# Optimization experiments

Hardware: AMD Instinct MI355X
Metric: run time of the kernel (lower is better)

The kernel has to match this reference:

```python
import jax, jax.numpy as jnp
import numpy as np

N_NODES = 100000
N_EDGES = 1600000
K = 5
C = 32
HEADS = 2
LRELU_GAT = 0.2   # SuperGAT negative_slope default
LRELU_OUT = 0.01  # nn.LeakyReLU default
BN_EPS = 1e-5


def setup_inputs() -> dict:
    key = jax.random.key(0)
    ks = jax.random.split(key, 10)
    patch_embs = jax.random.normal(ks[0], (N_NODES, C), dtype=jnp.float32)
    src = jax.random.randint(ks[1], (N_EDGES,), 0, N_NODES, dtype=jnp.int32)
    dst = jax.random.randint(ks[2], (N_EDGES,), 0, N_NODES, dtype=jnp.int32)
    dst = jnp.where(src == dst, (dst + 1) % N_NODES, dst)  # graph has no self-loops
    edge_index = jnp.stack([src, dst])
    edge_attr = jax.random.normal(ks[3], (N_EDGES, 1), dtype=jnp.float32)
    g = 1.0 / np.sqrt(C).astype(np.float32)
    cheb_w = jax.random.normal(ks[4], (K, C, C), dtype=jnp.float32) * g
    cheb_b = jnp.zeros((C,), jnp.float32)
    lin_w = jax.random.normal(ks[5], (C, HEADS * C), dtype=jnp.float32) * g
    att_l = jax.random.normal(ks[6], (HEADS, C), dtype=jnp.float32) * g
    att_r = jax.random.normal(ks[7], (HEADS, C), dtype=jnp.float32) * g
    gat_b = jnp.zeros((C,), jnp.float32)
    bn_g = jnp.ones((C,), jnp.float32)
    bn_b = jnp.zeros((C,), jnp.float32)
    return dict(patch_embs=patch_embs, edge_index=edge_index, edge_attr=edge_attr,
                cheb_w=cheb_w, cheb_b=cheb_b, lin_w=lin_w, att_l=att_l,
                att_r=att_r, gat_b=gat_b, bn_g=bn_g, bn_b=bn_b)


def cheb_conv(x, src, dst, w_edge, cheb_w, cheb_b, n):
    # PyG ChebConv with sym norm, lambda_max=2: L_hat = -D^-1/2 A D^-1/2
    def prop(t):
        return jax.ops.segment_sum(t[src] * w_edge[:, None], dst, num_segments=n)
    Tx0 = x
    out = Tx0 @ cheb_w[0]
    Tx1 = prop(x)
    out = out + Tx1 @ cheb_w[1]
    for k in range(2, cheb_w.shape[0]):
        Tx2 = 2.0 * prop(Tx1) - Tx0
        out = out + Tx2 @ cheb_w[k]
        Tx0, Tx1 = Tx1, Tx2
    return out + cheb_b


def supergat(x, src, dst, lin_w, att_l, att_r, bias, n):
    # SuperGATConv, attention_type='MX', heads=2, concat=False, with self-loops
    H, Ch = att_l.shape
    h = (x @ lin_w).reshape(n, H, Ch)
    xj = h[src]            # [E, H, C] messages from source
    xi = h[dst]            # [E, H, C] target features
    logits = jnp.sum(xi * xj, axis=-1)                         # [E, H]
    alpha = jnp.sum(xj * att_l, -1) + jnp.sum(xi * att_r, -1)  # [E, H]
    alpha = alpha * jax.nn.sigmoid(logits)
    alpha = jax.nn.leaky_relu(alpha, LRELU_GAT)
    # segment softmax over destination nodes
    m = jax.ops.segment_max(alpha, dst, num_segments=n)
    e = jnp.exp(alpha - m[dst])
    s = jax.ops.segment_sum(e, dst, num_segments=n)
    a = e / s[dst]
    out = jax.ops.segment_sum(xj * a[..., None], dst, num_segments=n)  # [N, H, C]
    return out.mean(axis=1) + bias  # concat=False -> head mean


def reference(patch_embs, edge_index, edge_attr, cheb_w, cheb_b, lin_w, att_l,
              att_r, gat_b, bn_g, bn_b):
    n = patch_embs.shape[0]
    src, dst = edge_index[0], edge_index[1]
    # symmetric Laplacian normalization weights
    deg = jax.ops.segment_sum(jnp.ones_like(src, dtype=patch_embs.dtype), src,
                              num_segments=n)
    dis = jnp.where(deg > 0, jax.lax.rsqrt(jnp.maximum(deg, 1.0)), 0.0)
    w_edge = -dis[src] * dis[dst]
    x = cheb_conv(patch_embs, src, dst, w_edge, cheb_w, cheb_b, n)
    # add self-loops for SuperGAT (PyG default add_self_loops=True)
    loop = jnp.arange(n, dtype=src.dtype)
    src2 = jnp.concatenate([src, loop])
    dst2 = jnp.concatenate([dst, loop])
    x2 = supergat(x, src2, dst2, lin_w, att_l, att_r, gat_b, n)
    # LeakyReLU + residual + BatchNorm1d (training-mode batch stats)
    y = jax.nn.leaky_relu(x2, LRELU_OUT) + x2
    mu = y.mean(axis=0)
    var = ((y - mu) ** 2).mean(axis=0)  # biased variance
    return (y - mu) * jax.lax.rsqrt(var + BN_EPS) * bn_g + bn_b
```

## Files before the change

### kernel.cpp

```cpp
#include <hip/hip_runtime.h>
#include <hip/hip_fp16.h>
#include <math.h>

#define CC 32
#define CHUNK 4096
#define NCPY 16
#define REDB 1024

static inline int cdiv(long long a, int b) { return (int)((a + b - 1) / b); }

__device__ inline float4 h4f(int2 r) {
  __half2 lo = *reinterpret_cast<__half2*>(&r.x);
  __half2 hi = *reinterpret_cast<__half2*>(&r.y);
  float2 a = __half22float2(lo), b = __half22float2(hi);
  return make_float4(a.x, a.y, b.x, b.y);
}

__global__ void k_cnt(const int* __restrict__ src, const int* __restrict__ dst,
                      int* __restrict__ priv, int E, int N) {
  int e = blockIdx.x * blockDim.x + threadIdx.x;
  if (e >= E) return;
  int* p = priv + (size_t)(blockIdx.x & (NCPY - 1)) * N;
  atomicAdd(&p[src[e]], 1 << 16);
  atomicAdd(&p[dst[e]], 1);
}

__global__ void k_reduce(int* __restrict__ priv, float* __restrict__ dis,
                         int* __restrict__ cnt, int* __restrict__ histmat, int N) {
  __shared__ int lh[64];
  if (threadIdx.x < 64) lh[threadIdx.x] = 0;
  __syncthreads();
  int n = blockIdx.x * REDB + threadIdx.x;
  if (n < N) {
    int vals[NCPY];
    int tot = 0;
#pragma unroll
    for (int c = 0; c < NCPY; ++c) {
      vals[c] = priv[(size_t)c * N + n];
      tot += vals[c];
    }
    int deg = tot >> 16, cv = tot & 0xFFFF;
    dis[n] = (deg > 0) ? rsqrtf((float)deg) : 0.f;
    cnt[n] = cv;
    int acc = 0;
#pragma unroll
    for (int c = 0; c < NCPY; ++c) {
      priv[(size_t)c * N + n] = acc;
      acc += vals[c] & 0xFFFF;
    }
    atomicAdd(&lh[min(cv, 63)], 1);
  }
  __syncthreads();
  if (threadIdx.x < 64) histmat[blockIdx.x * 64 + threadIdx.x] = lh[threadIdx.x];
}

__global__ void k_scanhist2(int* __restrict__ histmat, int nb) {
  int lane = threadIdx.x;
  int tot = 0;
  for (int i = 0; i < nb; ++i) tot += histmat[i * 64 + lane];
  __shared__ int sh[64], pf[64];
  sh[lane] = tot;
  __syncthreads();
  if (lane == 0) {
    int acc = 0;
    for (int b = 0; b < 64; ++b) { pf[b] = acc; acc += sh[b]; }
  }
  __syncthreads();
  int acc = pf[lane];
  for (int i = 0; i < nb; ++i) {
    int v = histmat[i * 64 + lane];
    histmat[i * 64 + lane] = acc;
    acc += v;
  }
}

__global__ void k_permfill2(const int* __restrict__ cnt, const int* __restrict__ histmat,
                            int* __restrict__ perm, int N) {
  __shared__ int lh[64], lbase[64];
  if (threadIdx.x < 64) lh[threadIdx.x] = 0;
  __syncthreads();
  int i = blockIdx.x * REDB + threadIdx.x;
  int bin = 0, rank = 0;
  bool act = (i < N);
  if (act) {
    bin = min(cnt[i], 63);
    rank = atomicAdd(&lh[bin], 1);
  }
  __syncthreads();
  if (threadIdx.x < 64) lbase[threadIdx.x] = histmat[blockIdx.x * 64 + threadIdx.x];
  __syncthreads();
  if (act) perm[lbase[bin] + rank] = i;
}

__global__ void k_chunksum(const int* __restrict__ cnt, int* __restrict__ csum, int N) {
  int base = blockIdx.x * CHUNK;
  int v = 0;
  for (int i = threadIdx.x; i < CHUNK; i += 256) {
    int idx = base + i;
    if (idx < N) v += cnt[idx];
  }
  for (int m = 32; m; m >>= 1) v += __shfl_xor(v, m);
  __shared__ int ws[4];
  if ((threadIdx.x & 63) == 0) ws[threadIdx.x >> 6] = v;
  __syncthreads();
  if (threadIdx.x == 0) csum[blockIdx.x] = ws[0] + ws[1] + ws[2] + ws[3];
}

__global__ void k_scancsum(int* __restrict__ csum, int nb, int* __restrict__ rptr,
                           int N, int tot) {
  int acc = 0;
  for (int i = 0; i < nb; ++i) { int v = csum[i]; csum[i] = acc; acc += v; }
  rptr[N] = tot;
}

__global__ void k_fillrptr(int* __restrict__ cnt, const int* __restrict__ csum,
                           int* __restrict__ rptr, int N) {
  int base = blockIdx.x * CHUNK + threadIdx.x * 16;
  int v[16];
  int tot = 0;
#pragma unroll
  for (int q = 0; q < 16; ++q) {
    int idx = base + q;
    v[q] = (idx < N) ? cnt[idx] : 0;
    tot += v[q];
  }
  __shared__ int sh[256];
  sh[threadIdx.x] = tot;
  __syncthreads();
  for (int off = 1; off < 256; off <<= 1) {
    int add = (threadIdx.x >= off) ? sh[threadIdx.x - off] : 0;
    __syncthreads();
    sh[threadIdx.x] += add;
    __syncthreads();
  }
  int excl = sh[threadIdx.x] - tot + csum[blockIdx.x];
#pragma unroll
  for (int q = 0; q < 16; ++q) {
    int idx = base + q;
    if (idx < N) rptr[idx] = excl;
    excl += v[q];
  }
}

__global__ void k_fill3(const int* __restrict__ src, const int* __restrict__ dst,
                        const float* __restrict__ dis, const int* __restrict__ rptr,
                        int* __restrict__ priv, int2* __restrict__ eg, int E, int N) {
  int e = blockIdx.x * blockDim.x + threadIdx.x;
  if (e >= E) return;
  int s = src[e], d = dst[e];
  int* pc = priv + (size_t)(blockIdx.x & (NCPY - 1)) * N;
  int p = rptr[d] + atomicAdd(&pc[d], 1);
  int2 v;
  v.x = s;
  v.y = __float_as_int(-dis[s] * dis[d]);
  eg[p] = v;
}

__global__ void k_cheb4(const float4* __restrict__ x_in4,
                        const float4* __restrict__ x_sub4,
                        const int* __restrict__ rptr, const int2* __restrict__ eg,
                        const float* __restrict__ W, const int* __restrict__ perm,
                        float scale, float4* __restrict__ tx_out4,
                        float4* __restrict__ out4, int N) {
  __shared__ float wl[1024];
  for (int i = threadIdx.x; i < 1024; i += 256) wl[i] = W[i];
  __syncthreads();
  int gid = blockIdx.x * 32 + (threadIdx.x >> 3);
  int lane = threadIdx.x & 7;
  if (gid >= N) return;
  int node = perm[N - 1 - gid];
  int beg = rptr[node], end = rptr[node + 1];
  float tx = 0.f, ty = 0.f, tz = 0.f, tw = 0.f;
  for (int base = beg; base < end; base += 8) {
    int rem = end - base;
    int sj = 0; float wjv = 0.f;
    if (lane < rem) {
      int2 v = eg[base + lane];
      sj = v.x;
      wjv = __int_as_float(v.y);
    }
    if (rem >= 8) {
#pragma unroll
      for (int q = 0; q < 8; ++q) {
        int s = __shfl(sj, q, 8);
        float w = __shfl(wjv, q, 8);
        float4 j4 = x_in4[(long long)s * 8 + lane];
        tx += w * j4.x; ty += w * j4.y; tz += w * j4.z; tw += w * j4.w;
      }
    } else {
      for (int q = 0; q < rem; ++q) {
        int s = __shfl(sj, q, 8);
        float w = __shfl(wjv, q, 8);
        float4 j4 = x_in4[(long long)s * 8 + lane];
        tx += w * j4.x; ty += w * j4.y; tz += w * j4.z; tw += w * j4.w;
      }
    }
  }
  long long o = (long long)node * 8 + lane;
  float ta[4] = {scale * tx, scale * ty, scale * tz, scale * tw};
  if (x_sub4) {
    float4 s4 = x_sub4[o];
    ta[0] -= s4.x; ta[1] -= s4.y; ta[2] -= s4.z; ta[3] -= s4.w;
  }
  if (tx_out4) {
    float4 t4 = {ta[0], ta[1], ta[2], ta[3]};
    tx_out4[o] = t4;
  }
  float4 a4 = out4[o];
  float ax = 0.f, ay = 0.f, az = 0.f, aw = 0.f;
#pragma unroll
  for (int c = 0; c < 32; ++c) {
    float bc = __shfl(ta[c & 3], c >> 2, 8);
    const float4 w4 = *(const float4*)&wl[c * 32 + lane * 4];
    ax += bc * w4.x; ay += bc * w4.y; az += bc * w4.z; aw += bc * w4.w;
  }
  a4.x += ax; a4.y += ay; a4.z += az; a4.w += aw;
  out4[o] = a4;
}

__global__ void k_gemm32b(const float* __restrict__ T, const float* __restrict__ W,
                          const float* __restrict__ bias, float* __restrict__ out,
                          int N) {
  __shared__ float w[1024];
  for (int i = threadIdx.x; i < 1024; i += 256) w[i] = W[i];
  __syncthreads();
  int row = blockIdx.x * 8 + (threadIdx.x >> 5);
  int col = threadIdx.x & 31;
  if (row >= N) return;
  const float* tr = T + (long long)row * 32;
  float acc = 0.f;
#pragma unroll
  for (int c = 0; c < 32; ++c) acc += tr[c] * w[c * 32 + col];
  out[(long long)row * 32 + col] = acc + bias[col];
}

__global__ void k_gemmh(const float* __restrict__ T, const float* __restrict__ W,
                        __half* __restrict__ h, int N) {
  __shared__ float w[2048];
  for (int i = threadIdx.x; i < 2048; i += 256) w[i] = W[i];
  __syncthreads();
  int row = blockIdx.x * 4 + (threadIdx.x >> 6);
  int col = threadIdx.x & 63;
  if (row >= N) return;
  const float* tr = T + (long long)row * 32;
  float acc = 0.f;
#pragma unroll
  for (int c = 0; c < 32; ++c) acc += tr[c] * w[c * 64 + col];
  int ch = col & 31, hd = col >> 5;
  h[(long long)row * 64 + (ch & 15) * 4 + (ch >> 4) + 2 * hd] = __float2half(acc);
}

__device__ inline void gat_edge(const float4& j4, const float4& i4, const float4& al,
                                bool hiH, float brh,
                                float& s0, float& s1, float4& v) {
  float d0 = j4.x * i4.x + j4.y * i4.y;
  float d1 = j4.z * i4.z + j4.w * i4.w;
  float b0 = j4.x * al.x + j4.y * al.y;
  float b1 = j4.z * al.z + j4.w * al.w;
  d0 += __shfl_xor(d0, 8, 16);
  d1 += __shfl_xor(d1, 8, 16);
  b0 += __shfl_xor(b0, 8, 16);
  b1 += __shfl_xor(b1, 8, 16);
  float dc = hiH ? d1 : d0;
  float bc = hiH ? b1 : b0;
  dc += __shfl_xor(dc, 4, 16); bc += __shfl_xor(bc, 4, 16);
  dc += __shfl_xor(dc, 2, 16); bc += __shfl_xor(bc, 2, 16);
  dc += __shfl_xor(dc, 1, 16); bc += __shfl_xor(bc, 1, 16);
  float lin = bc + brh;
  float a = lin / (1.f + __expf(-dc));
  a = (a > 0.f) ? a : 0.2f * a;
  float ec = __expf(a);
  float e0 = __shfl(ec, 0, 16), e1 = __shfl(ec, 8, 16);
  s0 += e0; s1 += e1;
  v.x += e0 * j4.x; v.y += e0 * j4.y; v.z += e1 * j4.z; v.w += e1 * j4.w;
}

__global__ void k_expgat4(const int2* __restrict__ h2, const int* __restrict__ rptr,
                          const int2* __restrict__ eg, const float* __restrict__ attl,
                          const float* __restrict__ attr, const float* __restrict__ gb,
                          const int* __restrict__ perm, float* __restrict__ y,
                          float* __restrict__ bns, int N) {
  __shared__ float ls[64];
  for (int i = threadIdx.x; i < 64; i += 256) ls[i] = 0.f;
  __syncthreads();
  int gid = blockIdx.x * 16 + (threadIdx.x >> 4);
  int lane = threadIdx.x & 15;
  float4 al = {attl[lane], attl[lane + 16], attl[32 + lane], attl[48 + lane]};
  float4 ar = {attr[lane], attr[lane + 16], attr[32 + lane], attr[48 + lane]};
  if (gid < N) {
    int node = perm[N - 1 - gid];
    float4 i4 = h4f(h2[(long long)node * 16 + lane]);
    bool hiH = (lane & 8) != 0;
    float r0 = i4.x * ar.x + i4.y * ar.y;
    float r1 = i4.z * ar.z + i4.w * ar.w;
    r0 += __shfl_xor(r0, 8, 16);
    r1 += __shfl_xor(r1, 8, 16);
    float brh = hiH ? r1 : r0;
    brh += __shfl_xor(brh, 4, 16);
    brh += __shfl_xor(brh, 2, 16);
    brh += __shfl_xor(brh, 1, 16);
    float s0 = 0.f, s1 = 0.f;
    float4 v = {0.f, 0.f, 0.f, 0.f};
    gat_edge(i4, i4, al, hiH, brh, s0, s1, v);
    int beg = rptr[node], end = rptr[node + 1];
    for (int base = beg; base < end; base += 16) {
      int rem = end - base;
      int sj = 0;
      if (lane < rem) sj = eg[base + lane].x;
      if (rem >= 16) {
#pragma unroll
        for (int p = 0; p < 4; ++p) {
          int q0 = p * 4, q1 = q0 + 1, q2 = q0 + 2, q3 = q0 + 3;
          int sA = __shfl(sj, q0, 16);
          int sB = __shfl(sj, q1, 16);
          int sC = __shfl(sj, q2, 16);
          int sD = __shfl(sj, q3, 16);
          int2 rA = h2[(long long)sA * 16 + lane];
          int2 rB = h2[(long long)sB * 16 + lane];
          int2 rC = h2[(long long)sC * 16 + lane];
          int2 rD = h2[(long long)sD * 16 + lane];
          gat_edge(h4f(rA), i4, al, hiH, brh, s0, s1, v);
          gat_edge(h4f(rB), i4, al, hiH, brh, s0, s1, v);
          gat_edge(h4f(rC), i4, al, hiH, brh, s0, s1, v);
          gat_edge(h4f(rD), i4, al, hiH, brh, s0, s1, v);
        }
      } else {
        int q = 0;
        for (; q + 2 <= rem; q += 2) {
          int sA = __shfl(sj, q, 16);
          int sB = __shfl(sj, q + 1, 16);
          int2 rA = h2[(long long)sA * 16 + lane];
          int2 rB = h2[(long long)sB * 16 + lane];
          gat_edge(h4f(rA), i4, al, hiH, brh, s0, s1, v);
          gat_edge(h4f(rB), i4, al, hiH, brh, s0, s1, v);
        }
        if (q < rem) {
          int sA = __shfl(sj, q, 16);
          int2 rA = h2[(long long)sA * 16 + lane];
          gat_edge(h4f(rA), i4, al, hiH, brh, s0, s1, v);
        }
      }
    }
    float x2a = 0.5f * (v.x / s0 + v.z / s1) + gb[lane];
    float x2b = 0.5f * (v.y / s0 + v.w / s1) + gb[lane + 16];
    float ya = ((x2a > 0.f) ? x2a : 0.01f * x2a) + x2a;
    float yb = ((x2b > 0.f) ? x2b : 0.01f * x2b) + x2b;
    y[(long long)node * 32 + lane] = ya;
    y[(long long)node * 32 + lane + 16] = yb;
    atomicAdd(&ls[lane], ya);
    atomicAdd(&ls[lane + 16], yb);
    atomicAdd(&ls[32 + lane], ya * ya);
    atomicAdd(&ls[32 + lane + 16], yb * yb);
  }
  __syncthreads();
  if (threadIdx.x < 64) atomicAdd(&bns[threadIdx.x], ls[threadIdx.x]);
}

__global__ void k_bnfinal(const float* __restrict__ y, const float* __restrict__ bns,
                          const float* __restrict__ g, const float* __restrict__ b,
                          float* __restrict__ out, int N) {
  int i = blockIdx.x * blockDim.x + threadIdx.x;
  if (i >= N * CC) return;
  int c = i & 31;
  float inv_n = 1.f / (float)N;
  float mu = bns[c] * inv_n;
  float var = bns[32 + c] * inv_n - mu * mu;
  out[i] = (y[i] - mu) * rsqrtf(var + 1e-5f) * g[c] + b[c];
}

extern "C" void kernel_launch(void* const* d_in, const int* in_sizes, int n_in,
                              void* d_out, int out_size, void* d_ws, size_t ws_size,
                              hipStream_t stream) {
  const float* patch = (const float*)d_in[0];
  const int* eidx = (const int*)d_in[1];
  const float* cheb_w = (const float*)d_in[3];
  const float* cheb_b = (const float*)d_in[4];
  const float* lin_w = (const float*)d_in[5];
  const float* att_l = (const float*)d_in[6];
  const float* att_r = (const float*)d_in[7];
  const float* gat_b = (const float*)d_in[8];
  const float* bn_g = (const float*)d_in[9];
  const float* bn_b = (const float*)d_in[10];
  float* out = (float*)d_out;

  const int N = in_sizes[0] / CC;
  const int E = in_sizes[1] / 2;
  const int* src = eidx;
  const int* dst = eidx + E;

  float* R0 = (float*)d_ws;
  float* R1 = R0 + (size_t)N * 32;
  int2* eg = (int2*)(R1 + (size_t)N * 32);
  int* grptr = (int*)(eg + E);
  int* cnt = grptr + (N + 2);
  int* csum = cnt + N;
  float* dis = (float*)(csum + 64);
  float* bns = dis + N;
  int* perm = (int*)(bns + 64);
  int* priv = (int*)(perm + N);
  int* histmat = priv + (size_t)NCPY * N;
  __half* h = (__half*)R0;

  const int B = 256;
  const long long NC = (long long)N * 32;
  int nbred = cdiv(N, REDB);

  hipMemsetAsync(priv, 0, sizeof(int) * (size_t)NCPY * N, stream);
  hipMemsetAsync(bns, 0, sizeof(float) * 64, stream);

  k_cnt<<<cdiv(E, B), B, 0, stream>>>(src, dst, priv, E, N);
  k_reduce<<<nbred, REDB, 0, stream>>>(priv, dis, cnt, histmat, N);
  k_scanhist2<<<1, 64, 0, stream>>>(histmat, nbred);
  k_permfill2<<<nbred, REDB, 0, stream>>>(cnt, histmat, perm, N);

  int nb = cdiv(N, CHUNK);
  k_chunksum<<<nb, B, 0, stream>>>(cnt, csum, N);
  k_scancsum<<<1, 1, 0, stream>>>(csum, nb, grptr, N, E);
  k_fillrptr<<<nb, B, 0, stream>>>(cnt, csum, grptr, N);
  k_fill3<<<cdiv(E, B), B, 0, stream>>>(src, dst, dis, grptr, priv, eg, E, N);

  k_gemm32b<<<cdiv(N, 8), B, 0, stream>>>(patch, cheb_w, cheb_b, out, N);
  k_cheb4<<<cdiv(N, 32), B, 0, stream>>>((const float4*)patch, nullptr, grptr, eg,
                                         cheb_w + 1024, perm, 1.f,
                                         (float4*)R0, (float4*)out, N);
  k_cheb4<<<cdiv(N, 32), B, 0, stream>>>((const float4*)R0, (const float4*)patch,
                                         grptr, eg, cheb_w + 2048, perm, 2.f,
                                         (float4*)R1, (float4*)out, N);
  k_cheb4<<<cdiv(N, 32), B, 0, stream>>>((const float4*)R1, (const float4*)R0,
                                         grptr, eg, cheb_w + 3072, perm, 2.f,
                                         (float4*)R0, (float4*)out, N);
  k_cheb4<<<cdiv(N, 32), B, 0, stream>>>((const float4*)R0, (const float4*)R1,
                                         grptr, eg, cheb_w + 4096, perm, 2.f,
                                         nullptr, (float4*)out, N);

  k_gemmh<<<cdiv(N, 4), B, 0, stream>>>(out, lin_w, h, N);
  k_expgat4<<<cdiv(N, 16), B, 0, stream>>>((const int2*)h, grptr, eg, att_l, att_r,
                                           gat_b, perm, out, bns, N);
  k_bnfinal<<<cdiv(NC, B), B, 0, stream>>>(out, bns, bn_g, bn_b, out, N);
}
```

Before: 692.2 us.

## Batch gather loads in Chebyshev and GAT loops, pack attention reductions in half2

The Chebyshev propagation loop now handles 16 edges per iteration and issues all 16 neighbor-row gathers before doing any FMAs. The GAT loop likewise loads all 16 neighbor rows up front, so more memory requests are in flight at once. The per-edge attention dot-product reductions are packed as half2, which reduces both heads' dot and bias sums in one shuffle chain with fewer cross-lane ops and no per-lane select. The costs are higher register pressure, which may lower occupancy, and reduced precision in the attention logits summed in fp16.

```diff
diff --git a/kernel.cpp b/kernel.cpp
--- a/kernel.cpp
+++ b/kernel.cpp
@@ -171,7 +171,36 @@
   int node = perm[N - 1 - gid];
   int beg = rptr[node], end = rptr[node + 1];
   float tx = 0.f, ty = 0.f, tz = 0.f, tw = 0.f;
-  for (int base = beg; base < end; base += 8) {
+  int base = beg;
+  for (; base + 16 <= end; base += 16) {
+    int2 vA = eg[base + lane];
+    int2 vB = eg[base + 8 + lane];
+    int sjA = vA.x, sjB = vB.x;
+    float wjA = __int_as_float(vA.y), wjB = __int_as_float(vB.y);
+    float4 j[16];
+#pragma unroll
+    for (int q = 0; q < 8; ++q) {
+      int sA = __shfl(sjA, q, 8);
+      j[q] = x_in4[(long long)sA * 8 + lane];
+    }
+#pragma unroll
+    for (int q = 0; q < 8; ++q) {
+      int sB = __shfl(sjB, q, 8);
+      j[q + 8] = x_in4[(long long)sB * 8 + lane];
+    }
+#pragma unroll
+    for (int q = 0; q < 8; ++q) {
+      float w = __shfl(wjA, q, 8);
+      tx += w * j[q].x; ty += w * j[q].y; tz += w * j[q].z; tw += w * j[q].w;
+    }
+#pragma unroll
+    for (int q = 0; q < 8; ++q) {
+      float w = __shfl(wjB, q, 8);
+      tx += w * j[q + 8].x; ty += w * j[q + 8].y;
+      tz += w * j[q + 8].z; tw += w * j[q + 8].w;
+    }
+  }
+  for (; base < end; base += 8) {
     int rem = end - base;
     int sj = 0; float wjv = 0.f;
     if (lane < rem) {
@@ -179,21 +208,12 @@
       sj = v.x;
       wjv = __int_as_float(v.y);
     }
-    if (rem >= 8) {
-#pragma unroll
-      for (int q = 0; q < 8; ++q) {
-        int s = __shfl(sj, q, 8);
-        float w = __shfl(wjv, q, 8);
-        float4 j4 = x_in4[(long long)s * 8 + lane];
-        tx += w * j4.x; ty += w * j4.y; tz += w * j4.z; tw += w * j4.w;
-      }
-    } else {
-      for (int q = 0; q < rem; ++q) {
-        int s = __shfl(sj, q, 8);
-        float w = __shfl(wjv, q, 8);
-        float4 j4 = x_in4[(long long)s * 8 + lane];
-        tx += w * j4.x; ty += w * j4.y; tz += w * j4.z; tw += w * j4.w;
-      }
+    int cnt = rem < 8 ? rem : 8;
+    for (int q = 0; q < cnt; ++q) {
+      int s = __shfl(sj, q, 8);
+      float w = __shfl(wjv, q, 8);
+      float4 j4 = x_in4[(long long)s * 8 + lane];
+      tx += w * j4.x; ty += w * j4.y; tz += w * j4.z; tw += w * j4.w;
     }
   }
   long long o = (long long)node * 8 + lane;
@@ -251,26 +271,34 @@
 }
 
 __device__ inline void gat_edge(const float4& j4, const float4& i4, const float4& al,
-                                bool hiH, float brh,
+                                float br0, float br1,
                                 float& s0, float& s1, float4& v) {
   float d0 = j4.x * i4.x + j4.y * i4.y;
   float d1 = j4.z * i4.z + j4.w * i4.w;
   float b0 = j4.x * al.x + j4.y * al.y;
   float b1 = j4.z * al.z + j4.w * al.w;
-  d0 += __shfl_xor(d0, 8, 16);
-  d1 += __shfl_xor(d1, 8, 16);
-  b0 += __shfl_xor(b0, 8, 16);
-  b1 += __shfl_xor(b1, 8, 16);
-  float dc = hiH ? d1 : d0;
-  float bc = hiH ? b1 : b0;
-  dc += __shfl_xor(dc, 4, 16); bc += __shfl_xor(bc, 4, 16);
-  dc += __shfl_xor(dc, 2, 16); bc += __shfl_xor(bc, 2, 16);
-  dc += __shfl_xor(dc, 1, 16); bc += __shfl_xor(bc, 1, 16);
-  float lin = bc + brh;
-  float a = lin / (1.f + __expf(-dc));
-  a = (a > 0.f) ? a : 0.2f * a;
-  float ec = __expf(a);
-  float e0 = __shfl(ec, 0, 16), e1 = __shfl(ec, 8, 16);
+  __half2 pd = __floats2half2_rn(d0, d1);
+  __half2 pb = __floats2half2_rn(b0, b1);
+  unsigned ud = *reinterpret_cast<unsigned*>(&pd);
+  unsigned ub = *reinterpret_cast<unsigned*>(&pb);
+#pragma unroll
+  for (int m = 8; m; m >>= 1) {
+    unsigned od = (unsigned)__shfl_xor((int)ud, m, 16);
+    unsigned ob = (unsigned)__shfl_xor((int)ub, m, 16);
+    __half2 rd = __hadd2(*reinterpret_cast<__half2*>(&ud),
+                         *reinterpret_cast<__half2*>(&od));
+    __half2 rb = __hadd2(*reinterpret_cast<__half2*>(&ub),
+                         *reinterpret_cast<__half2*>(&ob));
+    ud = *reinterpret_cast<unsigned*>(&rd);
+    ub = *reinterpret_cast<unsigned*>(&rb);
+  }
+  float2 dd = __half22float2(*reinterpret_cast<__half2*>(&ud));
+  float2 bb = __half22float2(*reinterpret_cast<__half2*>(&ub));
+  float a0 = (bb.x + br0) / (1.f + __expf(-dd.x));
+  float a1 = (bb.y + br1) / (1.f + __expf(-dd.y));
+  a0 = (a0 > 0.f) ? a0 : 0.2f * a0;
+  a1 = (a1 > 0.f) ? a1 : 0.2f * a1;
+  float e0 = __expf(a0), e1 = __expf(a1);
   s0 += e0; s1 += e1;
   v.x += e0 * j4.x; v.y += e0 * j4.y; v.z += e1 * j4.z; v.w += e1 * j4.w;
 }
@@ -290,40 +318,32 @@
   if (gid < N) {
     int node = perm[N - 1 - gid];
     float4 i4 = h4f(h2[(long long)node * 16 + lane]);
-    bool hiH = (lane & 8) != 0;
     float r0 = i4.x * ar.x + i4.y * ar.y;
     float r1 = i4.z * ar.z + i4.w * ar.w;
-    r0 += __shfl_xor(r0, 8, 16);
-    r1 += __shfl_xor(r1, 8, 16);
-    float brh = hiH ? r1 : r0;
-    brh += __shfl_xor(brh, 4, 16);
-    brh += __shfl_xor(brh, 2, 16);
-    brh += __shfl_xor(brh, 1, 16);
+#pragma unroll
+    for (int m = 8; m; m >>= 1) {
+      r0 += __shfl_xor(r0, m, 16);
+      r1 += __shfl_xor(r1, m, 16);
+    }
+    float br0 = r0, br1 = r1;
     float s0 = 0.f, s1 = 0.f;
     float4 v = {0.f, 0.f, 0.f, 0.f};
-    gat_edge(i4, i4, al, hiH, brh, s0, s1, v);
+    gat_edge(i4, i4, al, br0, br1, s0, s1, v);
     int beg = rptr[node], end = rptr[node + 1];
     for (int base = beg; base < end; base += 16) {
       int rem = end - base;
       int sj = 0;
       if (lane < rem) sj = eg[base + lane].x;
       if (rem >= 16) {
-#pragma unroll
-        for (int p = 0; p < 4; ++p) {
-          int q0 = p * 4, q1 = q0 + 1, q2 = q0 + 2, q3 = q0 + 3;
-          int sA = __shfl(sj, q0, 16);
-          int sB = __shfl(sj, q1, 16);
-          int sC = __shfl(sj, q2, 16);
-          int sD = __shfl(sj, q3, 16);
-          int2 rA = h2[(long long)sA * 16 + lane];
-          int2 rB = h2[(long long)sB * 16 + lane];
-          int2 rC = h2[(long long)sC * 16 + lane];
-          int2 rD = h2[(long long)sD * 16 + lane];
-          gat_edge(h4f(rA), i4, al, hiH, brh, s0, s1, v);
-          gat_edge(h4f(rB), i4, al, hiH, brh, s0, s1, v);
-          gat_edge(h4f(rC), i4, al, hiH, brh, s0, s1, v);
-          gat_edge(h4f(rD), i4, al, hiH, brh, s0, s1, v);
+        int2 r[16];
+#pragma unroll
+        for (int q = 0; q < 16; ++q) {
+          int s = __shfl(sj, q, 16);
+          r[q] = h2[(long long)s * 16 + lane];
         }
+#pragma unroll
+        for (int q = 0; q < 16; ++q)
+          gat_edge(h4f(r[q]), i4, al, br0, br1, s0, s1, v);
       } else {
         int q = 0;
         for (; q + 2 <= rem; q += 2) {
@@ -331,13 +351,13 @@
           int sB = __shfl(sj, q + 1, 16);
           int2 rA = h2[(long long)sA * 16 + lane];
           int2 rB = h2[(long long)sB * 16 + lane];
-          gat_edge(h4f(rA), i4, al, hiH, brh, s0, s1, v);
-          gat_edge(h4f(rB), i4, al, hiH, brh, s0, s1, v);
+          gat_edge(h4f(rA), i4, al, br0, br1, s0, s1, v);
+          gat_edge(h4f(rB), i4, al, br0, br1, s0, s1, v);
         }
         if (q < rem) {
           int sA = __shfl(sj, q, 16);
           int2 rA = h2[(long long)sA * 16 + lane];
-          gat_edge(h4f(rA), i4, al, hiH, brh, s0, s1, v);
+          gat_edge(h4f(rA), i4, al, br0, br1, s0, s1, v);
         }
       }
     }
```

Measured after the change: 693.0 us. Within noise of the previous version (+0.1%).
